# Performance work log

Measured on AMD Instinct MI355X. Metric: run time of the kernel, lower is better.

The kernel has to match this reference:

```python
import jax, jax.numpy as jnp
import numpy as np

B, S, HID = 2, 2048, 1024
NH, DK, DV = 4, 256, 256   # head_k_dim = head_v_dim = 1024 / 4
KSZ = 4                    # conv_size
EPS = 1e-5


def causal_conv1d(x, w):
    # x: [B, S, C] channels-last, w: [C, K] depthwise kernel (torch [C,1,K] squeezed)
    K = w.shape[1]
    Sn = x.shape[1]
    xp = jnp.pad(x, ((0, 0), (K - 1, 0), (0, 0)))
    # cross-correlation with left padding K-1 -> causal: out[t] = sum_j w[:,j] * x[t-(K-1)+j]
    out = xp[:, 0:Sn, :] * w[:, 0]
    for j in range(1, K):
        out = out + xp[:, j:j + Sn, :] * w[:, j]
    return out


def l2norm(x, eps=1e-6):
    return x * jax.lax.rsqrt(jnp.sum(x * x, axis=-1, keepdims=True) + eps)


def rms_norm(x, w, eps=EPS):
    return x * jax.lax.rsqrt(jnp.mean(x * x, axis=-1, keepdims=True) + eps) * w


def delta_rule(q, k, v, beta):
    # q,k: [B,S,H,dk]; v: [B,S,H,dv]; beta: [B,S,H]
    Bn, Sn, Hn, dk = q.shape
    dv = v.shape[-1]
    N = Bn * Hn
    qs = jnp.moveaxis(q, 1, 0).reshape(Sn, N, dk)
    ks = jnp.moveaxis(k, 1, 0).reshape(Sn, N, dk)
    vs = jnp.moveaxis(v, 1, 0).reshape(Sn, N, dv)
    bs = jnp.moveaxis(beta, 1, 0).reshape(Sn, N)

    S0 = jnp.zeros((N, dk, dv), q.dtype)

    def step(St, inp):
        qt, kt, vt, bt = inp
        kS = jnp.einsum('nk,nkv->nv', kt, St)              # k^T S
        St = St + jnp.einsum('nk,nv->nkv', kt, bt[:, None] * (vt - kS))
        ot = jnp.einsum('nk,nkv->nv', qt, St)
        return St, ot

    _, o = jax.lax.scan(step, S0, (qs, ks, vs, bs))        # o: [S, N, dv]
    o = o.reshape(Sn, Bn, Hn, dv)
    return jnp.moveaxis(o, 0, 1)                            # [B,S,H,dv]


def setup_inputs() -> dict:
    key = jax.random.key(0)
    ks = jax.random.split(key, 10)
    w_scale = 2.0 ** (-2.5) * np.sqrt(6.0 / (HID + HID))   # xavier_uniform with gain 2^-2.5
    u = lambda k, shp, s: jax.random.uniform(k, shp, jnp.float32, -s, s)
    return {
        'hidden_states': jax.random.normal(ks[0], (B, S, HID), jnp.float32),
        'Wq': u(ks[1], (HID, NH * DK), w_scale),
        'Wk': u(ks[2], (HID, NH * DK), w_scale),
        'Wv': u(ks[3], (HID, NH * DV), w_scale),
        'Wb': u(ks[4], (HID, NH), w_scale),
        'conv_q': jax.random.normal(ks[5], (NH * DK, KSZ), jnp.float32) * 0.2,
        'conv_k': jax.random.normal(ks[6], (NH * DK, KSZ), jnp.float32) * 0.2,
        'conv_v': jax.random.normal(ks[7], (NH * DV, KSZ), jnp.float32) * 0.2,
        'norm_w': jnp.ones((DV,), jnp.float32),
        'Wo': u(ks[8], (NH * DV, HID), w_scale),
    }


def reference(hidden_states, Wq, Wk, Wv, Wb, conv_q, conv_k, conv_v, norm_w, Wo):
    q = hidden_states @ Wq                                  # [B,S,key_dim]
    k = hidden_states @ Wk
    v = hidden_states @ Wv
    q = causal_conv1d(q, conv_q)
    k = causal_conv1d(k, conv_k)
    v = causal_conv1d(v, conv_v)
    q = jax.nn.silu(q).reshape(B, S, NH, DK)
    k = jax.nn.silu(k).reshape(B, S, NH, DK)
    v = jax.nn.silu(v).reshape(B, S, NH, DV)
    beta = jax.nn.sigmoid(hidden_states @ Wb)               # [B,S,H]
    q = l2norm(q)
    k = l2norm(k)
    o = delta_rule(q, k, v, beta)                           # [B,S,H,dv]
    o = rms_norm(o, norm_w)
    o = o.reshape(B, S, NH * DV) @ Wo                       # [B,S,HID]
    return o
```

## Files before the change

kernel.cpp:

```cpp
#include <hip/hip_runtime.h>
#include <math.h>

#define BB   2
#define SS   2048
#define HIDD 1024
#define ROWS 4096
#define NCH  32
#define CH   64

typedef unsigned short u16t;
typedef unsigned int   u32t;

typedef __attribute__((ext_vector_type(8))) short bf16x8;
typedef __attribute__((ext_vector_type(4))) float f32x4;

__device__ __forceinline__ float bf2f(u16t u) { return __uint_as_float(((u32t)u) << 16); }
__device__ __forceinline__ u16t f2bf(float f) {
    u32t b = __float_as_uint(f);
    return (u16t)((b + 0x7FFFu + ((b >> 16) & 1u)) >> 16);
}
__device__ __forceinline__ float lo_bf(u32t u) { return __uint_as_float(u << 16); }
__device__ __forceinline__ float hi_bf(u32t u) { return __uint_as_float(u & 0xFFFF0000u); }

__device__ __forceinline__ float waveReduceSum(float v) {
#pragma unroll
    for (int m = 1; m < 64; m <<= 1) v += __shfl_xor(v, m, 64);
    return v;
}

__device__ __forceinline__ void gload16(const void* g, void* l) {
    __builtin_amdgcn_global_load_lds(
        (const __attribute__((address_space(1))) unsigned int*)g,
        (__attribute__((address_space(3))) unsigned int*)l, 16, 0, 0);
}

#define MFMA(a, b, c) __builtin_amdgcn_mfma_f32_16x16x32_bf16(a, b, c, 0, 0, 0)

__global__ __launch_bounds__(256) void f2bf_kernel(const float* __restrict__ in,
                                                   u16t* __restrict__ out) {
    const size_t idx = ((size_t)blockIdx.x * 256 + threadIdx.x) * 8;
    float4 a = *(const float4*)&in[idx];
    float4 b = *(const float4*)&in[idx + 4];
    ushort4 o1, o2;
    o1.x = f2bf(a.x); o1.y = f2bf(a.y); o1.z = f2bf(a.z); o1.w = f2bf(a.w);
    o2.x = f2bf(b.x); o2.y = f2bf(b.y); o2.z = f2bf(b.z); o2.w = f2bf(b.w);
    *(ushort4*)&out[idx] = o1;
    *(ushort4*)&out[idx + 4] = o2;
}

__global__ __launch_bounds__(256) void transpose_w(const float* __restrict__ W,
                                                   u16t* __restrict__ WT) {
    __shared__ u16t tile[64][65];
    const int t = threadIdx.x;
    const int r0 = blockIdx.y * 64, c0 = blockIdx.x * 64;
    const int lr = t >> 2, lc4 = (t & 3) * 16;
#pragma unroll
    for (int m = 0; m < 4; ++m) {
        float4 v = *(const float4*)&W[(size_t)(r0 + lr) * 1024 + c0 + lc4 + m * 4];
        tile[lr][lc4 + m * 4 + 0] = f2bf(v.x);
        tile[lr][lc4 + m * 4 + 1] = f2bf(v.y);
        tile[lr][lc4 + m * 4 + 2] = f2bf(v.z);
        tile[lr][lc4 + m * 4 + 3] = f2bf(v.w);
    }
    __syncthreads();
#pragma unroll
    for (int m = 0; m < 16; ++m)
        WT[(size_t)(c0 + lr) * 1024 + r0 + lc4 + m] = tile[lc4 + m][lr];
}

__global__ __launch_bounds__(256) void gemm_mfma(const u16t* __restrict__ A,
                                                 const u16t* __restrict__ BT,
                                                 float* __restrict__ Cf,
                                                 u16t* __restrict__ Cb, int obf,
                                                 int M, int N, int K) {
    __shared__ u16t As[128 * 64];
    __shared__ u16t Bs[128 * 64];
    const int t = threadIdx.x, l = t & 63, w = t >> 6;
    const int wr = w >> 1, wc = w & 1;
    const int rowBase = blockIdx.y * 128, colBase = blockIdx.x * 128;
    const int l15 = l & 15, g4 = l >> 4;

    const int srow = l >> 3;
    const int sj = (l & 7) ^ srow;
    const u16t* aSrc = A + (size_t)(rowBase + srow) * K + sj * 8;
    const u16t* bSrc = BT + (size_t)(colBase + srow) * K + sj * 8;

    f32x4 acc[4][4];
#pragma unroll
    for (int i = 0; i < 4; ++i)
#pragma unroll
        for (int j = 0; j < 4; ++j) acc[i][j] = (f32x4){0.f, 0.f, 0.f, 0.f};

    for (int k0 = 0; k0 < K; k0 += 64) {
#pragma unroll
        for (int i = 0; i < 4; ++i) {
            const int rb = (i * 4 + w) * 8;
            gload16(aSrc + (size_t)rb * K + k0, &As[rb * 64]);
            gload16(bSrc + (size_t)rb * K + k0, &Bs[rb * 64]);
        }
        __syncthreads();
#pragma unroll
        for (int kh = 0; kh < 2; ++kh) {
            bf16x8 aF[4], bF[4];
#pragma unroll
            for (int mi = 0; mi < 4; ++mi) {
                const int row = wr * 64 + mi * 16 + l15;
                const int phys = (kh * 4 + g4) ^ (row & 7);
                aF[mi] = *(const bf16x8*)&As[row * 64 + phys * 8];
            }
#pragma unroll
            for (int ni = 0; ni < 4; ++ni) {
                const int row = wc * 64 + ni * 16 + l15;
                const int phys = (kh * 4 + g4) ^ (row & 7);
                bF[ni] = *(const bf16x8*)&Bs[row * 64 + phys * 8];
            }
#pragma unroll
            for (int mi = 0; mi < 4; ++mi)
#pragma unroll
                for (int ni = 0; ni < 4; ++ni)
                    acc[mi][ni] = MFMA(aF[mi], bF[ni], acc[mi][ni]);
        }
        __syncthreads();
    }
#pragma unroll
    for (int mi = 0; mi < 4; ++mi)
#pragma unroll
        for (int ni = 0; ni < 4; ++ni)
#pragma unroll
            for (int rg = 0; rg < 4; ++rg) {
                const int row = rowBase + wr * 64 + mi * 16 + g4 * 4 + rg;
                const int col = colBase + wc * 64 + ni * 16 + l15;
                const float v = acc[mi][ni][rg];
                if (obf) Cb[(size_t)row * N + col] = f2bf(v);
                else     Cf[(size_t)row * N + col] = v;
            }
}

__global__ __launch_bounds__(256) void beta_kernel(const float* __restrict__ X,
                                                   const float* __restrict__ Wb,
                                                   float* __restrict__ beta) {
    const int gw   = (blockIdx.x * blockDim.x + threadIdx.x) >> 6;
    const int lane = threadIdx.x & 63;
    if (gw >= ROWS) return;
    const float* x = X + (size_t)gw * HIDD;
    float a0 = 0.f, a1 = 0.f, a2 = 0.f, a3 = 0.f;
#pragma unroll
    for (int i = 0; i < 4; ++i) {
        const int k = lane * 16 + i * 4;
        float4 xv = *(const float4*)&x[k];
        float4 w0 = *(const float4*)&Wb[(size_t)(k + 0) * 4];
        float4 w1 = *(const float4*)&Wb[(size_t)(k + 1) * 4];
        float4 w2 = *(const float4*)&Wb[(size_t)(k + 2) * 4];
        float4 w3 = *(const float4*)&Wb[(size_t)(k + 3) * 4];
        a0 += xv.x * w0.x + xv.y * w1.x + xv.z * w2.x + xv.w * w3.x;
        a1 += xv.x * w0.y + xv.y * w1.y + xv.z * w2.y + xv.w * w3.y;
        a2 += xv.x * w0.z + xv.y * w1.z + xv.z * w2.z + xv.w * w3.z;
        a3 += xv.x * w0.w + xv.y * w1.w + xv.z * w2.w + xv.w * w3.w;
    }
    a0 = waveReduceSum(a0); a1 = waveReduceSum(a1);
    a2 = waveReduceSum(a2); a3 = waveReduceSum(a3);
    if (lane == 0) {
        float4 o = make_float4(1.f / (1.f + expf(-a0)), 1.f / (1.f + expf(-a1)),
                               1.f / (1.f + expf(-a2)), 1.f / (1.f + expf(-a3)));
        *(float4*)&beta[(size_t)gw * 4] = o;
    }
}

__global__ __launch_bounds__(256) void conv_bf16(const u16t* __restrict__ in,
                                                 const float* __restrict__ w,
                                                 u16t* __restrict__ out, int doL2) {
    const int gw   = (blockIdx.x * blockDim.x + threadIdx.x) >> 6;
    const int lane = threadIdx.x & 63;
    const int r = gw >> 2;
    const int h = gw & 3;
    const int b = r >> 11;
    const int s = r & 2047;
    const int c4 = h * 256 + lane * 4;

    const float4 wr0 = *(const float4*)&w[(size_t)(c4 + 0) * 4];
    const float4 wr1 = *(const float4*)&w[(size_t)(c4 + 1) * 4];
    const float4 wr2 = *(const float4*)&w[(size_t)(c4 + 2) * 4];
    const float4 wr3 = *(const float4*)&w[(size_t)(c4 + 3) * 4];

    const size_t rowB = (size_t)(b << 11);
    float x0[4] = {0, 0, 0, 0}, x1[4] = {0, 0, 0, 0}, x2[4] = {0, 0, 0, 0}, x3[4];
    ushort4 u;
    if (s >= 3) { u = *(const ushort4*)&in[(rowB + s - 3) * HIDD + c4];
        x0[0] = bf2f(u.x); x0[1] = bf2f(u.y); x0[2] = bf2f(u.z); x0[3] = bf2f(u.w); }
    if (s >= 2) { u = *(const ushort4*)&in[(rowB + s - 2) * HIDD + c4];
        x1[0] = bf2f(u.x); x1[1] = bf2f(u.y); x1[2] = bf2f(u.z); x1[3] = bf2f(u.w); }
    if (s >= 1) { u = *(const ushort4*)&in[(rowB + s - 1) * HIDD + c4];
        x2[0] = bf2f(u.x); x2[1] = bf2f(u.y); x2[2] = bf2f(u.z); x2[3] = bf2f(u.w); }
    u = *(const ushort4*)&in[(rowB + s) * HIDD + c4];
    x3[0] = bf2f(u.x); x3[1] = bf2f(u.y); x3[2] = bf2f(u.z); x3[3] = bf2f(u.w);

    float y0 = wr0.x * x0[0] + wr0.y * x1[0] + wr0.z * x2[0] + wr0.w * x3[0];
    float y1 = wr1.x * x0[1] + wr1.y * x1[1] + wr1.z * x2[1] + wr1.w * x3[1];
    float y2 = wr2.x * x0[2] + wr2.y * x1[2] + wr2.z * x2[2] + wr2.w * x3[2];
    float y3 = wr3.x * x0[3] + wr3.y * x1[3] + wr3.z * x2[3] + wr3.w * x3[3];

    y0 = y0 / (1.f + expf(-y0)); y1 = y1 / (1.f + expf(-y1));
    y2 = y2 / (1.f + expf(-y2)); y3 = y3 / (1.f + expf(-y3));

    if (doL2) {
        float ss = y0 * y0 + y1 * y1 + y2 * y2 + y3 * y3;
        ss = waveReduceSum(ss);
        float sc = rsqrtf(ss + 1e-6f);
        y0 *= sc; y1 *= sc; y2 *= sc; y3 *= sc;
    }
    ushort4 o;
    o.x = f2bf(y0); o.y = f2bf(y1); o.z = f2bf(y2); o.w = f2bf(y3);
    *(ushort4*)&out[(size_t)r * HIDD + c4] = o;
}

__global__ __launch_bounds__(256) void conv_k_chunk(const u16t* __restrict__ pre,
                                                    const float* __restrict__ w,
                                                    u16t* __restrict__ rowout,
                                                    u16t* __restrict__ trout) {
    const int t = threadIdx.x;
    const int bh = blockIdx.x >> 5, c = blockIdx.x & 31;
    const int b = bh >> 2, h = bh & 3;
    const int i = t >> 2, g = t & 3;
    const int s = c * 64 + i;
    const size_t row = (size_t)b * 2048 + s;
    const int ch0 = h * 256 + g * 64;
    const int cloc = g * 64;
    float y[64];
#pragma unroll
    for (int m = 0; m < 8; ++m) {
        const int cm = ch0 + m * 8;
        uint4 x3 = *(const uint4*)&pre[row * 1024 + cm];
        uint4 x2 = (s >= 1) ? *(const uint4*)&pre[(row - 1) * 1024 + cm] : make_uint4(0, 0, 0, 0);
        uint4 x1 = (s >= 2) ? *(const uint4*)&pre[(row - 2) * 1024 + cm] : make_uint4(0, 0, 0, 0);
        uint4 x0 = (s >= 3) ? *(const uint4*)&pre[(row - 3) * 1024 + cm] : make_uint4(0, 0, 0, 0);
        u32t c0[4] = {x0.x, x0.y, x0.z, x0.w};
        u32t c1[4] = {x1.x, x1.y, x1.z, x1.w};
        u32t c2[4] = {x2.x, x2.y, x2.z, x2.w};
        u32t c3[4] = {x3.x, x3.y, x3.z, x3.w};
#pragma unroll
        for (int p = 0; p < 4; ++p) {
            const int ch = m * 8 + p * 2;
            float4 wA = *(const float4*)&w[(size_t)(ch0 + ch) * 4];
            float4 wB = *(const float4*)&w[(size_t)(ch0 + ch + 1) * 4];
            float ya = wA.x * lo_bf(c0[p]) + wA.y * lo_bf(c1[p]) + wA.z * lo_bf(c2[p]) + wA.w * lo_bf(c3[p]);
            float yb = wB.x * hi_bf(c0[p]) + wB.y * hi_bf(c1[p]) + wB.z * hi_bf(c2[p]) + wB.w * hi_bf(c3[p]);
            ya = ya / (1.f + expf(-ya));
            yb = yb / (1.f + expf(-yb));
            y[ch] = ya; y[ch + 1] = yb;
        }
    }
    float ss = 0.f;
#pragma unroll
    for (int e = 0; e < 64; ++e) ss += y[e] * y[e];
    ss += __shfl_xor(ss, 1);
    ss += __shfl_xor(ss, 2);
    const float sc = rsqrtf(ss + 1e-6f);
#pragma unroll
    for (int m = 0; m < 8; ++m) {
        uint4 o;
        u32t* op = (u32t*)&o;
#pragma unroll
        for (int p = 0; p < 4; ++p) {
            u16t a = f2bf(y[m * 8 + p * 2] * sc);
            u16t bb2 = f2bf(y[m * 8 + p * 2 + 1] * sc);
            op[p] = (u32t)a | ((u32t)bb2 << 16);
        }
        *(uint4*)&rowout[row * 1024 + ch0 + m * 8] = o;
    }
#pragma unroll
    for (int e = 0; e < 64; ++e)
        trout[((size_t)bh * 256 + cloc + e) * 2048 + s] = f2bf(y[e] * sc);
}

__global__ __launch_bounds__(256) void prep_kernel(const u16t* __restrict__ qcb,
                                                   const u16t* __restrict__ kcb,
                                                   const float* __restrict__ beta,
                                                   u16t* __restrict__ Tghi,
                                                   u16t* __restrict__ Tglo,
                                                   u16t* __restrict__ Agb) {
    __shared__ float KT[256][68];
    __shared__ float QT[256][68];
    __shared__ float Af[64][68];
    const int t = threadIdx.x;
    const int bhc = blockIdx.x;
    const int bh = bhc >> 5, c = bhc & 31;
    const int b = bh >> 2, h = bh & 3;
    const int tb = b * SS + c * CH;

    {
        const int i = t & 63, rb = t >> 6;
        const u16t* kg = kcb + (size_t)(tb + i) * HIDD + h * 256 + rb * 64;
        const u16t* qg = qcb + (size_t)(tb + i) * HIDD + h * 256 + rb * 64;
#pragma unroll
        for (int m = 0; m < 8; ++m) {
            uint4 kv = ((const uint4*)kg)[m];
            uint4 qv = ((const uint4*)qg)[m];
            u32t kw[4] = {kv.x, kv.y, kv.z, kv.w};
            u32t qw[4] = {qv.x, qv.y, qv.z, qv.w};
#pragma unroll
            for (int n = 0; n < 4; ++n) {
                int rr = rb * 64 + m * 8 + n * 2;
                KT[rr][i]     = lo_bf(kw[n]);
                KT[rr + 1][i] = hi_bf(kw[n]);
                QT[rr][i]     = lo_bf(qw[n]);
                QT[rr + 1][i] = hi_bf(qw[n]);
            }
        }
    }
    __syncthreads();

    const int it = t & 63, jb = t >> 6;
    float kk[16], qk[16];
#pragma unroll
    for (int m = 0; m < 16; ++m) { kk[m] = 0.f; qk[m] = 0.f; }
#pragma unroll 2
    for (int r = 0; r < 256; ++r) {
        float ki = KT[r][it];
        float qi = QT[r][it];
        float4 ka = *(const float4*)&KT[r][jb * 16 + 0];
        float4 kb = *(const float4*)&KT[r][jb * 16 + 4];
        float4 kc = *(const float4*)&KT[r][jb * 16 + 8];
        float4 kd = *(const float4*)&KT[r][jb * 16 + 12];
        float kj[16] = {ka.x, ka.y, ka.z, ka.w, kb.x, kb.y, kb.z, kb.w,
                        kc.x, kc.y, kc.z, kc.w, kd.x, kd.y, kd.z, kd.w};
#pragma unroll
        for (int m = 0; m < 16; ++m) { kk[m] += ki * kj[m]; qk[m] += qi * kj[m]; }
    }

    const float bta = beta[(size_t)(tb + it) * 4 + h];
    u16t* ag = Agb + (size_t)bhc * 4096 + (size_t)it * 64 + jb * 16;
#pragma unroll
    for (int m = 0; m < 16; ++m) {
        int j = jb * 16 + m;
        Af[it][j] = (j < it) ? bta * kk[m] : 0.f;
    }
#pragma unroll
    for (int m4 = 0; m4 < 4; ++m4) {
        ushort4 o;
        o.x = f2bf((jb * 16 + m4 * 4 + 0 <= it) ? qk[m4 * 4 + 0] : 0.f);
        o.y = f2bf((jb * 16 + m4 * 4 + 1 <= it) ? qk[m4 * 4 + 1] : 0.f);
        o.z = f2bf((jb * 16 + m4 * 4 + 2 <= it) ? qk[m4 * 4 + 2] : 0.f);
        o.w = f2bf((jb * 16 + m4 * 4 + 3 <= it) ? qk[m4 * 4 + 3] : 0.f);
        *(ushort4*)&ag[m4 * 4] = o;
    }
    __syncthreads();

    if (t < 64) {
        const int ccol = t;
        float tc[64];
#pragma unroll
        for (int j = 0; j < 64; ++j) tc[j] = (j == ccol) ? 1.f : 0.f;
#pragma unroll
        for (int i = 1; i < 64; ++i) {
            float a = 0.f;
#pragma unroll
            for (int j = 0; j < i; ++j) a += Af[i][j] * tc[j];
            tc[i] -= a;
        }
        u16t* th = Tghi + (size_t)bhc * 4096;
        u16t* tl = Tglo + (size_t)bhc * 4096;
#pragma unroll
        for (int i = 0; i < 64; ++i) {
            u16t hi = f2bf(tc[i]);
            th[i * 64 + ccol] = hi;
            tl[i * 64 + ccol] = f2bf(tc[i] - bf2f(hi));
        }
    }
}

__global__ __launch_bounds__(256) void scan_mfma(const u16t* __restrict__ qcb,
                                                 const u16t* __restrict__ kcb,
                                                 const u16t* __restrict__ ktr,
                                                 const u16t* __restrict__ vcb,
                                                 const float* __restrict__ beta,
                                                 const u16t* __restrict__ TghiG,
                                                 const u16t* __restrict__ TgloG,
                                                 const u16t* __restrict__ AgbG,
                                                 u16t* __restrict__ o_raw) {
    __shared__ u16t Kr[64 * 256];
    __shared__ u16t Qr[64 * 256];
    __shared__ u16t Kc[256 * 64];
    __shared__ u16t Shi[16 * 256];
    __shared__ u16t Slo[16 * 256];
    __shared__ u16t Thi[64 * 64];
    __shared__ u16t Tlo[64 * 64];
    __shared__ u16t Atb[64 * 64];
    __shared__ u16t Rhi[16 * 64];
    __shared__ u16t Rlo[16 * 64];
    __shared__ u16t Uhi[16 * 64];
    __shared__ u16t Ulo[16 * 64];

    const int t = threadIdx.x, l = t & 63, w = t >> 6;
    const int bh = blockIdx.x >> 4, vt = blockIdx.x & 15;
    const int b = bh >> 2, h = bh & 3;
    const int vcol0 = vt * 16;
    const int vlow = l & 15, g4 = l >> 4;
    const int td0 = 16 * w + 4 * g4;

    for (int i = t; i < 16 * 256; i += 256) { Shi[i] = 0; Slo[i] = 0; }
    f32x4 sf[4];
#pragma unroll
    for (int q = 0; q < 4; ++q) sf[q] = (f32x4){0.f, 0.f, 0.f, 0.f};
    __syncthreads();

    for (int c = 0; c < NCH; ++c) {
        const int trow0 = b * 2048 + c * 64;
        const int bhc = bh * 32 + c;

        {
            const int lr2 = l >> 5, s5 = l & 31;
            const u16t* kB = kcb + (size_t)trow0 * 1024 + h * 256;
            const u16t* qB = qcb + (size_t)trow0 * 1024 + h * 256;
#pragma unroll
            for (int i = 0; i < 8; ++i) {
                const int tb2 = (i * 4 + w) * 2;
                const int tr = tb2 + lr2;
                const int j = s5 ^ (tr & 7);
                gload16(kB + (size_t)tr * 1024 + j * 8, &Kr[tb2 * 256]);
                gload16(qB + (size_t)tr * 1024 + j * 8, &Qr[tb2 * 256]);
            }
            const int lr8 = l >> 3, s3 = l & 7;
#pragma unroll
            for (int i = 0; i < 8; ++i) {
                const int rb = (i * 4 + w) * 8;
                const int r = rb + lr8;
                const int j = s3 ^ lr8;
                gload16(ktr + ((size_t)bh * 256 + r) * 2048 + (c * 64 + j * 8), &Kc[rb * 64]);
            }
#pragma unroll
            for (int i = 0; i < 2; ++i) {
                const int rb = (i * 4 + w) * 8;
                const int r = rb + lr8;
                const int j = s3 ^ lr8;
                gload16(TghiG + (size_t)bhc * 4096 + r * 64 + j * 8, &Thi[rb * 64]);
                gload16(TgloG + (size_t)bhc * 4096 + r * 64 + j * 8, &Tlo[rb * 64]);
                gload16(AgbG + (size_t)bhc * 4096 + r * 64 + j * 8, &Atb[rb * 64]);
            }
        }
        float vf[4], bta[4];
#pragma unroll
        for (int rg = 0; rg < 4; ++rg) {
            vf[rg]  = bf2f(vcb[(size_t)(trow0 + td0 + rg) * 1024 + h * 256 + vcol0 + vlow]);
            bta[rg] = beta[(size_t)(trow0 + td0 + rg) * 4 + h];
        }
        __syncthreads();

        f32x4 Wacc = (f32x4){0.f, 0.f, 0.f, 0.f};
        f32x4 O1   = (f32x4){0.f, 0.f, 0.f, 0.f};
        const int arow = 16 * w + vlow;
#pragma unroll
        for (int ks = 0; ks < 8; ++ks) {
            const int physA = (4 * ks + g4) ^ (arow & 7);
            const int physB = (4 * ks + g4) ^ (vlow & 7);
            bf16x8 aK = *(const bf16x8*)&Kr[arow * 256 + physA * 8];
            bf16x8 aQ = *(const bf16x8*)&Qr[arow * 256 + physA * 8];
            bf16x8 bH = *(const bf16x8*)&Shi[vlow * 256 + physB * 8];
            bf16x8 bL = *(const bf16x8*)&Slo[vlow * 256 + physB * 8];
            Wacc = MFMA(aK, bH, Wacc); Wacc = MFMA(aK, bL, Wacc);
            O1   = MFMA(aQ, bH, O1);   O1   = MFMA(aQ, bL, O1);
        }
        {
            u16t rh[4], rl[4];
#pragma unroll
            for (int rg = 0; rg < 4; ++rg) {
                float rv = bta[rg] * (vf[rg] - Wacc[rg]);
                u16t hi = f2bf(rv);
                rh[rg] = hi;
                rl[rg] = f2bf(rv - bf2f(hi));
            }
            const int tslot = 2 * w + (g4 >> 1);
            const int base = vlow * 64 + ((tslot ^ (vlow & 7)) << 3) + ((g4 & 1) << 2);
            uint2 ph, pl;
            ph.x = (u32t)rh[0] | ((u32t)rh[1] << 16); ph.y = (u32t)rh[2] | ((u32t)rh[3] << 16);
            pl.x = (u32t)rl[0] | ((u32t)rl[1] << 16); pl.y = (u32t)rl[2] | ((u32t)rl[3] << 16);
            *(uint2*)&Rhi[base] = ph;
            *(uint2*)&Rlo[base] = pl;
        }
        __syncthreads();

        f32x4 Uacc = (f32x4){0.f, 0.f, 0.f, 0.f};
#pragma unroll
        for (int ks = 0; ks < 2; ++ks) {
            const int physA = (4 * ks + g4) ^ (arow & 7);
            const int physB = (4 * ks + g4) ^ (vlow & 7);
            bf16x8 aH = *(const bf16x8*)&Thi[arow * 64 + physA * 8];
            bf16x8 aL = *(const bf16x8*)&Tlo[arow * 64 + physA * 8];
            bf16x8 bH = *(const bf16x8*)&Rhi[vlow * 64 + physB * 8];
            bf16x8 bL = *(const bf16x8*)&Rlo[vlow * 64 + physB * 8];
            Uacc = MFMA(aH, bH, Uacc);
            Uacc = MFMA(aH, bL, Uacc);
            Uacc = MFMA(aL, bH, Uacc);
        }
        {
            u16t uh[4], ul[4];
#pragma unroll
            for (int rg = 0; rg < 4; ++rg) {
                u16t hi = f2bf(Uacc[rg]);
                uh[rg] = hi;
                ul[rg] = f2bf(Uacc[rg] - bf2f(hi));
            }
            const int tslot = 2 * w + (g4 >> 1);
            const int base = vlow * 64 + ((tslot ^ (vlow & 7)) << 3) + ((g4 & 1) << 2);
            uint2 ph, pl;
            ph.x = (u32t)uh[0] | ((u32t)uh[1] << 16); ph.y = (u32t)uh[2] | ((u32t)uh[3] << 16);
            pl.x = (u32t)ul[0] | ((u32t)ul[1] << 16); pl.y = (u32t)ul[2] | ((u32t)ul[3] << 16);
            *(uint2*)&Uhi[base] = ph;
            *(uint2*)&Ulo[base] = pl;
        }
        __syncthreads();

        bf16x8 uhf[2], ulf[2];
#pragma unroll
        for (int ks = 0; ks < 2; ++ks) {
            const int physB = (4 * ks + g4) ^ (vlow & 7);
            uhf[ks] = *(const bf16x8*)&Uhi[vlow * 64 + physB * 8];
            ulf[ks] = *(const bf16x8*)&Ulo[vlow * 64 + physB * 8];
        }
        f32x4 Oacc = O1;
#pragma unroll
        for (int ks = 0; ks < 2; ++ks) {
            const int physA = (4 * ks + g4) ^ (arow & 7);
            bf16x8 aA = *(const bf16x8*)&Atb[arow * 64 + physA * 8];
            Oacc = MFMA(aA, uhf[ks], Oacc);
            Oacc = MFMA(aA, ulf[ks], Oacc);
        }
#pragma unroll
        for (int rg = 0; rg < 4; ++rg)
            o_raw[(size_t)(trow0 + td0 + rg) * 1024 + h * 256 + vcol0 + vlow] = f2bf(Oacc[rg]);

#pragma unroll
        for (int q = 0; q < 4; ++q) {
            const int rrow = 64 * w + 16 * q + vlow;
#pragma unroll
            for (int ks = 0; ks < 2; ++ks) {
                const int physA = (4 * ks + g4) ^ (rrow & 7);
                bf16x8 aC = *(const bf16x8*)&Kc[rrow * 64 + physA * 8];
                sf[q] = MFMA(aC, uhf[ks], sf[q]);
                sf[q] = MFMA(aC, ulf[ks], sf[q]);
            }
        }
#pragma unroll
        for (int q = 0; q < 4; ++q) {
            u16t sh[4], sl[4];
#pragma unroll
            for (int rg = 0; rg < 4; ++rg) {
                u16t hi = f2bf(sf[q][rg]);
                sh[rg] = hi;
                sl[rg] = f2bf(sf[q][rg] - bf2f(hi));
            }
            const int rslot = 8 * w + 2 * q + (g4 >> 1);
            const int base = vlow * 256 + ((rslot ^ (vlow & 7)) << 3) + ((g4 & 1) << 2);
            uint2 ph, pl;
            ph.x = (u32t)sh[0] | ((u32t)sh[1] << 16); ph.y = (u32t)sh[2] | ((u32t)sh[3] << 16);
            pl.x = (u32t)sl[0] | ((u32t)sl[1] << 16); pl.y = (u32t)sl[2] | ((u32t)sl[3] << 16);
            *(uint2*)&Shi[base] = ph;
            *(uint2*)&Slo[base] = pl;
        }
        __syncthreads();
    }
}

__global__ __launch_bounds__(256) void rms_kernel(const u16t* __restrict__ in,
                                                  const float* __restrict__ w,
                                                  u16t* __restrict__ out) {
    const int gw   = (blockIdx.x * blockDim.x + threadIdx.x) >> 6;
    const int lane = threadIdx.x & 63;
    const int r = gw >> 2;
    const int h = gw & 3;
    const size_t base = (size_t)r * HIDD + h * 256 + lane * 4;
    ushort4 xv = *(const ushort4*)&in[base];
    float x0 = bf2f(xv.x), x1 = bf2f(xv.y), x2 = bf2f(xv.z), x3 = bf2f(xv.w);
    float ss = x0 * x0 + x1 * x1 + x2 * x2 + x3 * x3;
    ss = waveReduceSum(ss);
    const float sc = rsqrtf(ss * (1.0f / 256.0f) + 1e-5f);
    float4 wv = *(const float4*)&w[lane * 4];
    ushort4 o;
    o.x = f2bf(x0 * sc * wv.x); o.y = f2bf(x1 * sc * wv.y);
    o.z = f2bf(x2 * sc * wv.z); o.w = f2bf(x3 * sc * wv.w);
    *(ushort4*)&out[base] = o;
}

extern "C" void kernel_launch(void* const* d_in, const int* in_sizes, int n_in,
                              void* d_out, int out_size, void* d_ws, size_t ws_size,
                              hipStream_t stream) {
    const float* X      = (const float*)d_in[0];
    const float* Wq     = (const float*)d_in[1];
    const float* Wk     = (const float*)d_in[2];
    const float* Wv     = (const float*)d_in[3];
    const float* Wb     = (const float*)d_in[4];
    const float* conv_q = (const float*)d_in[5];
    const float* conv_k = (const float*)d_in[6];
    const float* conv_v = (const float*)d_in[7];
    const float* norm_w = (const float*)d_in[8];
    const float* Wo     = (const float*)d_in[9];
    float* out = (float*)d_out;

    char* W8 = (char*)d_ws;
    const size_t MB = 1u << 20;
    u16t* Xbf   = (u16t*)(W8 + 0 * MB);
    u16t* o_raw = Xbf;
    u16t* qpre  = (u16t*)(W8 + 8 * MB);
    u16t* o_nrm = qpre;
    u16t* kpre  = (u16t*)(W8 + 16 * MB);
    u16t* Tghi  = (u16t*)(W8 + 16 * MB);
    u16t* Tglo  = (u16t*)(W8 + 18 * MB);
    u16t* Agb   = (u16t*)(W8 + 20 * MB);
    u16t* vpre  = (u16t*)(W8 + 24 * MB);
    u16t* ktr   = (u16t*)(W8 + 24 * MB);
    u16t* WqT   = (u16t*)(W8 + 32 * MB);
    u16t* qcb   = (u16t*)(W8 + 32 * MB);
    u16t* WkT   = (u16t*)(W8 + 40 * MB);
    u16t* kcb   = (u16t*)(W8 + 40 * MB);
    u16t* WvT   = (u16t*)(W8 + 48 * MB);
    u16t* vcb   = (u16t*)(W8 + 48 * MB);
    u16t* WoT   = (u16t*)(W8 + 56 * MB);
    float* betab = (float*)(W8 + 58 * MB);

    dim3 tgrid(16, 16);
    f2bf_kernel<<<2048, 256, 0, stream>>>(X, Xbf);
    transpose_w<<<tgrid, 256, 0, stream>>>(Wq, WqT);
    transpose_w<<<tgrid, 256, 0, stream>>>(Wk, WkT);
    transpose_w<<<tgrid, 256, 0, stream>>>(Wv, WvT);
    transpose_w<<<tgrid, 256, 0, stream>>>(Wo, WoT);

    dim3 ggrid(HIDD / 128, ROWS / 128);
    gemm_mfma<<<ggrid, 256, 0, stream>>>(Xbf, WqT, nullptr, qpre, 1, ROWS, HIDD, HIDD);
    gemm_mfma<<<ggrid, 256, 0, stream>>>(Xbf, WkT, nullptr, kpre, 1, ROWS, HIDD, HIDD);
    gemm_mfma<<<ggrid, 256, 0, stream>>>(Xbf, WvT, nullptr, vpre, 1, ROWS, HIDD, HIDD);
    beta_kernel<<<ROWS / 4, 256, 0, stream>>>(X, Wb, betab);

    conv_bf16<<<ROWS, 256, 0, stream>>>(vpre, conv_v, vcb, 0);
    conv_bf16<<<ROWS, 256, 0, stream>>>(qpre, conv_q, qcb, 1);
    conv_k_chunk<<<256, 256, 0, stream>>>(kpre, conv_k, kcb, ktr);

    prep_kernel<<<256, 256, 0, stream>>>(qcb, kcb, betab, Tghi, Tglo, Agb);
    scan_mfma<<<128, 256, 0, stream>>>(qcb, kcb, ktr, vcb, betab, Tghi, Tglo, Agb, o_raw);

    rms_kernel<<<ROWS, 256, 0, stream>>>(o_raw, norm_w, o_nrm);
    gemm_mfma<<<ggrid, 256, 0, stream>>>(o_nrm, WoT, out, nullptr, 0, ROWS, HIDD, HIDD);
}
```

Measured before the change: 316.4 us.

## Prefetch scan operands into registers and merge QKV projections into one GEMM

The chunked delta-rule scan kernel no longer stages K, Q, K-transpose, T and A tiles through shared memory. Each wave now loads its MFMA fragments straight into registers and prefetches the next chunk's operands during the current chunk's compute, so global latency overlaps with MFMA work and several barriers' worth of LDS traffic go away. The three Q/K/V projection GEMMs become one launch with 768 blocks by passing plane strides, relying on the three transposed weights and outputs sitting 8 MB apart. This raises register pressure (launch_bounds 256,1) and depends on that buffer layout staying contiguous.

```diff
diff --git a/kernel.cpp b/kernel.cpp
--- a/kernel.cpp
+++ b/kernel.cpp
@@ -72,7 +72,8 @@
                                                  const u16t* __restrict__ BT,
                                                  float* __restrict__ Cf,
                                                  u16t* __restrict__ Cb, int obf,
-                                                 int M, int N, int K) {
+                                                 int M, int N, int K,
+                                                 size_t bStrideP, size_t cStrideP) {
     __shared__ u16t As[128 * 64];
     __shared__ u16t Bs[128 * 64];
     const int t = threadIdx.x, l = t & 63, w = t >> 6;
@@ -80,10 +81,13 @@
     const int rowBase = blockIdx.y * 128, colBase = blockIdx.x * 128;
     const int l15 = l & 15, g4 = l >> 4;
 
+    const int bplane = colBase >> 10;
+    const int bcol = colBase & 1023;
+
     const int srow = l >> 3;
     const int sj = (l & 7) ^ srow;
     const u16t* aSrc = A + (size_t)(rowBase + srow) * K + sj * 8;
-    const u16t* bSrc = BT + (size_t)(colBase + srow) * K + sj * 8;
+    const u16t* bSrc = BT + (size_t)bplane * bStrideP + (size_t)(bcol + srow) * K + sj * 8;
 
     f32x4 acc[4][4];
 #pragma unroll
@@ -130,9 +134,10 @@
             for (int rg = 0; rg < 4; ++rg) {
                 const int row = rowBase + wr * 64 + mi * 16 + g4 * 4 + rg;
                 const int col = colBase + wc * 64 + ni * 16 + l15;
+                const int plane = col >> 10, cc = col & 1023;
                 const float v = acc[mi][ni][rg];
-                if (obf) Cb[(size_t)row * N + col] = f2bf(v);
-                else     Cf[(size_t)row * N + col] = v;
+                if (obf) Cb[(size_t)plane * cStrideP + (size_t)row * 1024 + cc] = f2bf(v);
+                else     Cf[(size_t)plane * cStrideP + (size_t)row * 1024 + cc] = v;
             }
 }
 
@@ -368,23 +373,17 @@
     }
 }
 
-__global__ __launch_bounds__(256) void scan_mfma(const u16t* __restrict__ qcb,
-                                                 const u16t* __restrict__ kcb,
-                                                 const u16t* __restrict__ ktr,
-                                                 const u16t* __restrict__ vcb,
-                                                 const float* __restrict__ beta,
-                                                 const u16t* __restrict__ TghiG,
-                                                 const u16t* __restrict__ TgloG,
-                                                 const u16t* __restrict__ AgbG,
-                                                 u16t* __restrict__ o_raw) {
-    __shared__ u16t Kr[64 * 256];
-    __shared__ u16t Qr[64 * 256];
-    __shared__ u16t Kc[256 * 64];
+__global__ __launch_bounds__(256, 1) void scan_mfma(const u16t* __restrict__ qcb,
+                                                    const u16t* __restrict__ kcb,
+                                                    const u16t* __restrict__ ktr,
+                                                    const u16t* __restrict__ vcb,
+                                                    const float* __restrict__ beta,
+                                                    const u16t* __restrict__ TghiG,
+                                                    const u16t* __restrict__ TgloG,
+                                                    const u16t* __restrict__ AgbG,
+                                                    u16t* __restrict__ o_raw) {
     __shared__ u16t Shi[16 * 256];
     __shared__ u16t Slo[16 * 256];
-    __shared__ u16t Thi[64 * 64];
-    __shared__ u16t Tlo[64 * 64];
-    __shared__ u16t Atb[64 * 64];
     __shared__ u16t Rhi[16 * 64];
     __shared__ u16t Rlo[16 * 64];
     __shared__ u16t Uhi[16 * 64];
@@ -395,150 +394,146 @@
     const int b = bh >> 2, h = bh & 3;
     const int vcol0 = vt * 16;
     const int vlow = l & 15, g4 = l >> 4;
-    const int td0 = 16 * w + 4 * g4;
 
     for (int i = t; i < 16 * 256; i += 256) { Shi[i] = 0; Slo[i] = 0; }
     f32x4 sf[4];
 #pragma unroll
     for (int q = 0; q < 4; ++q) sf[q] = (f32x4){0.f, 0.f, 0.f, 0.f};
+
+    bf16x8 kf[8], qf[8], tfh[2], tfl[2], af[2], kcf[8];
+    u16t vfb[4];
+    float bta[4];
+
+    auto loadKQ = [&](int c) {
+        const size_t rb = (size_t)(b * 2048 + c * 64 + 16 * w + vlow) * 1024 + h * 256 + g4 * 8;
+#pragma unroll
+        for (int ks = 0; ks < 8; ++ks) {
+            kf[ks] = *(const bf16x8*)(kcb + rb + ks * 32);
+            qf[ks] = *(const bf16x8*)(qcb + rb + ks * 32);
+        }
+    };
+    auto loadVB = [&](int c) {
+        const int r0 = b * 2048 + c * 64 + 16 * w + 4 * g4;
+#pragma unroll
+        for (int rg = 0; rg < 4; ++rg) {
+            vfb[rg] = vcb[(size_t)(r0 + rg) * 1024 + h * 256 + vcol0 + vlow];
+            bta[rg] = beta[(size_t)(r0 + rg) * 4 + h];
+        }
+    };
+    auto loadT = [&](int c) {
+        const size_t tb2 = (size_t)(bh * 32 + c) * 4096 + (size_t)(16 * w + vlow) * 64 + g4 * 8;
+        tfh[0] = *(const bf16x8*)(TghiG + tb2);
+        tfh[1] = *(const bf16x8*)(TghiG + tb2 + 32);
+        tfl[0] = *(const bf16x8*)(TgloG + tb2);
+        tfl[1] = *(const bf16x8*)(TgloG + tb2 + 32);
+    };
+    auto loadA = [&](int c) {
+        const size_t tb2 = (size_t)(bh * 32 + c) * 4096 + (size_t)(16 * w + vlow) * 64 + g4 * 8;
+        af[0] = *(const bf16x8*)(AgbG + tb2);
+        af[1] = *(const bf16x8*)(AgbG + tb2 + 32);
+    };
+    auto loadKC = [&](int c) {
+        const size_t cb2 = ((size_t)bh * 256 + 64 * w + vlow) * 2048 + c * 64 + g4 * 8;
+#pragma unroll
+        for (int q2 = 0; q2 < 4; ++q2) {
+            kcf[q2 * 2 + 0] = *(const bf16x8*)(ktr + cb2 + (size_t)(16 * q2) * 2048);
+            kcf[q2 * 2 + 1] = *(const bf16x8*)(ktr + cb2 + (size_t)(16 * q2) * 2048 + 32);
+        }
+    };
+
+    loadKQ(0); loadVB(0); loadT(0); loadA(0); loadKC(0);
     __syncthreads();
 
     for (int c = 0; c < NCH; ++c) {
+        const int cn = (c + 1 < NCH) ? c + 1 : c;
         const int trow0 = b * 2048 + c * 64;
-        const int bhc = bh * 32 + c;
-
-        {
-            const int lr2 = l >> 5, s5 = l & 31;
-            const u16t* kB = kcb + (size_t)trow0 * 1024 + h * 256;
-            const u16t* qB = qcb + (size_t)trow0 * 1024 + h * 256;
-#pragma unroll
-            for (int i = 0; i < 8; ++i) {
-                const int tb2 = (i * 4 + w) * 2;
-                const int tr = tb2 + lr2;
-                const int j = s5 ^ (tr & 7);
-                gload16(kB + (size_t)tr * 1024 + j * 8, &Kr[tb2 * 256]);
-                gload16(qB + (size_t)tr * 1024 + j * 8, &Qr[tb2 * 256]);
-            }
-            const int lr8 = l >> 3, s3 = l & 7;
-#pragma unroll
-            for (int i = 0; i < 8; ++i) {
-                const int rb = (i * 4 + w) * 8;
-                const int r = rb + lr8;
-                const int j = s3 ^ lr8;
-                gload16(ktr + ((size_t)bh * 256 + r) * 2048 + (c * 64 + j * 8), &Kc[rb * 64]);
-            }
-#pragma unroll
-            for (int i = 0; i < 2; ++i) {
-                const int rb = (i * 4 + w) * 8;
-                const int r = rb + lr8;
-                const int j = s3 ^ lr8;
-                gload16(TghiG + (size_t)bhc * 4096 + r * 64 + j * 8, &Thi[rb * 64]);
-                gload16(TgloG + (size_t)bhc * 4096 + r * 64 + j * 8, &Tlo[rb * 64]);
-                gload16(AgbG + (size_t)bhc * 4096 + r * 64 + j * 8, &Atb[rb * 64]);
-            }
-        }
-        float vf[4], bta[4];
-#pragma unroll
-        for (int rg = 0; rg < 4; ++rg) {
-            vf[rg]  = bf2f(vcb[(size_t)(trow0 + td0 + rg) * 1024 + h * 256 + vcol0 + vlow]);
-            bta[rg] = beta[(size_t)(trow0 + td0 + rg) * 4 + h];
-        }
-        __syncthreads();
 
         f32x4 Wacc = (f32x4){0.f, 0.f, 0.f, 0.f};
         f32x4 O1   = (f32x4){0.f, 0.f, 0.f, 0.f};
-        const int arow = 16 * w + vlow;
 #pragma unroll
         for (int ks = 0; ks < 8; ++ks) {
-            const int physA = (4 * ks + g4) ^ (arow & 7);
-            const int physB = (4 * ks + g4) ^ (vlow & 7);
-            bf16x8 aK = *(const bf16x8*)&Kr[arow * 256 + physA * 8];
-            bf16x8 aQ = *(const bf16x8*)&Qr[arow * 256 + physA * 8];
-            bf16x8 bH = *(const bf16x8*)&Shi[vlow * 256 + physB * 8];
-            bf16x8 bL = *(const bf16x8*)&Slo[vlow * 256 + physB * 8];
-            Wacc = MFMA(aK, bH, Wacc); Wacc = MFMA(aK, bL, Wacc);
-            O1   = MFMA(aQ, bH, O1);   O1   = MFMA(aQ, bL, O1);
+            const int pb = (((ks * 4 + g4) ^ (vlow & 7)) << 3);
+            bf16x8 bH = *(const bf16x8*)&Shi[vlow * 256 + pb];
+            bf16x8 bL = *(const bf16x8*)&Slo[vlow * 256 + pb];
+            Wacc = MFMA(kf[ks], bH, Wacc); Wacc = MFMA(kf[ks], bL, Wacc);
+            O1   = MFMA(qf[ks], bH, O1);   O1   = MFMA(qf[ks], bL, O1);
         }
         {
-            u16t rh[4], rl[4];
-#pragma unroll
-            for (int rg = 0; rg < 4; ++rg) {
-                float rv = bta[rg] * (vf[rg] - Wacc[rg]);
-                u16t hi = f2bf(rv);
-                rh[rg] = hi;
-                rl[rg] = f2bf(rv - bf2f(hi));
-            }
             const int tslot = 2 * w + (g4 >> 1);
             const int base = vlow * 64 + ((tslot ^ (vlow & 7)) << 3) + ((g4 & 1) << 2);
+            u16t rh[4], rl[4];
+#pragma unroll
+            for (int rg = 0; rg < 4; ++rg) {
+                float rv = bta[rg] * (bf2f(vfb[rg]) - Wacc[rg]);
+                rh[rg] = f2bf(rv);
+                rl[rg] = f2bf(rv - bf2f(rh[rg]));
+            }
             uint2 ph, pl;
             ph.x = (u32t)rh[0] | ((u32t)rh[1] << 16); ph.y = (u32t)rh[2] | ((u32t)rh[3] << 16);
             pl.x = (u32t)rl[0] | ((u32t)rl[1] << 16); pl.y = (u32t)rl[2] | ((u32t)rl[3] << 16);
             *(uint2*)&Rhi[base] = ph;
             *(uint2*)&Rlo[base] = pl;
         }
+        loadKQ(cn);
+        loadVB(cn);
         __syncthreads();
 
         f32x4 Uacc = (f32x4){0.f, 0.f, 0.f, 0.f};
 #pragma unroll
         for (int ks = 0; ks < 2; ++ks) {
-            const int physA = (4 * ks + g4) ^ (arow & 7);
-            const int physB = (4 * ks + g4) ^ (vlow & 7);
-            bf16x8 aH = *(const bf16x8*)&Thi[arow * 64 + physA * 8];
-            bf16x8 aL = *(const bf16x8*)&Tlo[arow * 64 + physA * 8];
-            bf16x8 bH = *(const bf16x8*)&Rhi[vlow * 64 + physB * 8];
-            bf16x8 bL = *(const bf16x8*)&Rlo[vlow * 64 + physB * 8];
-            Uacc = MFMA(aH, bH, Uacc);
-            Uacc = MFMA(aH, bL, Uacc);
-            Uacc = MFMA(aL, bH, Uacc);
+            const int pb = (((ks * 4 + g4) ^ (vlow & 7)) << 3);
+            bf16x8 bH = *(const bf16x8*)&Rhi[vlow * 64 + pb];
+            bf16x8 bL = *(const bf16x8*)&Rlo[vlow * 64 + pb];
+            Uacc = MFMA(tfh[ks], bH, Uacc);
+            Uacc = MFMA(tfh[ks], bL, Uacc);
+            Uacc = MFMA(tfl[ks], bH, Uacc);
         }
         {
-            u16t uh[4], ul[4];
-#pragma unroll
-            for (int rg = 0; rg < 4; ++rg) {
-                u16t hi = f2bf(Uacc[rg]);
-                uh[rg] = hi;
-                ul[rg] = f2bf(Uacc[rg] - bf2f(hi));
-            }
             const int tslot = 2 * w + (g4 >> 1);
             const int base = vlow * 64 + ((tslot ^ (vlow & 7)) << 3) + ((g4 & 1) << 2);
+            u16t uh[4], ul[4];
+#pragma unroll
+            for (int rg = 0; rg < 4; ++rg) {
+                uh[rg] = f2bf(Uacc[rg]);
+                ul[rg] = f2bf(Uacc[rg] - bf2f(uh[rg]));
+            }
             uint2 ph, pl;
             ph.x = (u32t)uh[0] | ((u32t)uh[1] << 16); ph.y = (u32t)uh[2] | ((u32t)uh[3] << 16);
             pl.x = (u32t)ul[0] | ((u32t)ul[1] << 16); pl.y = (u32t)ul[2] | ((u32t)ul[3] << 16);
             *(uint2*)&Uhi[base] = ph;
             *(uint2*)&Ulo[base] = pl;
         }
+        loadT(cn);
         __syncthreads();
 
         bf16x8 uhf[2], ulf[2];
 #pragma unroll
         for (int ks = 0; ks < 2; ++ks) {
-            const int physB = (4 * ks + g4) ^ (vlow & 7);
-            uhf[ks] = *(const bf16x8*)&Uhi[vlow * 64 + physB * 8];
-            ulf[ks] = *(const bf16x8*)&Ulo[vlow * 64 + physB * 8];
+            const int pb = (((ks * 4 + g4) ^ (vlow & 7)) << 3);
+            uhf[ks] = *(const bf16x8*)&Uhi[vlow * 64 + pb];
+            ulf[ks] = *(const bf16x8*)&Ulo[vlow * 64 + pb];
         }
         f32x4 Oacc = O1;
 #pragma unroll
         for (int ks = 0; ks < 2; ++ks) {
-            const int physA = (4 * ks + g4) ^ (arow & 7);
-            bf16x8 aA = *(const bf16x8*)&Atb[arow * 64 + physA * 8];
-            Oacc = MFMA(aA, uhf[ks], Oacc);
-            Oacc = MFMA(aA, ulf[ks], Oacc);
+            Oacc = MFMA(af[ks], uhf[ks], Oacc);
+            Oacc = MFMA(af[ks], ulf[ks], Oacc);
         }
 #pragma unroll
         for (int rg = 0; rg < 4; ++rg)
-            o_raw[(size_t)(trow0 + td0 + rg) * 1024 + h * 256 + vcol0 + vlow] = f2bf(Oacc[rg]);
+            o_raw[(size_t)(trow0 + 16 * w + 4 * g4 + rg) * 1024 + h * 256 + vcol0 + vlow] = f2bf(Oacc[rg]);
+        loadA(cn);
 
 #pragma unroll
         for (int q = 0; q < 4; ++q) {
-            const int rrow = 64 * w + 16 * q + vlow;
 #pragma unroll
             for (int ks = 0; ks < 2; ++ks) {
-                const int physA = (4 * ks + g4) ^ (rrow & 7);
-                bf16x8 aC = *(const bf16x8*)&Kc[rrow * 64 + physA * 8];
-                sf[q] = MFMA(aC, uhf[ks], sf[q]);
-                sf[q] = MFMA(aC, ulf[ks], sf[q]);
-            }
-        }
+                sf[q] = MFMA(kcf[q * 2 + ks], uhf[ks], sf[q]);
+                sf[q] = MFMA(kcf[q * 2 + ks], ulf[ks], sf[q]);
+            }
+        }
+        loadKC(cn);
+
 #pragma unroll
         for (int q = 0; q < 4; ++q) {
             u16t sh[4], sl[4];
@@ -616,6 +611,8 @@
     u16t* WoT   = (u16t*)(W8 + 56 * MB);
     float* betab = (float*)(W8 + 58 * MB);
 
+    const size_t PL = 4194304;
+
     dim3 tgrid(16, 16);
     f2bf_kernel<<<2048, 256, 0, stream>>>(X, Xbf);
     transpose_w<<<tgrid, 256, 0, stream>>>(Wq, WqT);
@@ -623,10 +620,8 @@
     transpose_w<<<tgrid, 256, 0, stream>>>(Wv, WvT);
     transpose_w<<<tgrid, 256, 0, stream>>>(Wo, WoT);
 
-    dim3 ggrid(HIDD / 128, ROWS / 128);
-    gemm_mfma<<<ggrid, 256, 0, stream>>>(Xbf, WqT, nullptr, qpre, 1, ROWS, HIDD, HIDD);
-    gemm_mfma<<<ggrid, 256, 0, stream>>>(Xbf, WkT, nullptr, kpre, 1, ROWS, HIDD, HIDD);
-    gemm_mfma<<<ggrid, 256, 0, stream>>>(Xbf, WvT, nullptr, vpre, 1, ROWS, HIDD, HIDD);
+    gemm_mfma<<<dim3(24, 32), 256, 0, stream>>>(Xbf, WqT, nullptr, qpre, 1,
+                                                ROWS, 3072, HIDD, PL, PL);
     beta_kernel<<<ROWS / 4, 256, 0, stream>>>(X, Wb, betab);
 
     conv_bf16<<<ROWS, 256, 0, stream>>>(vpre, conv_v, vcb, 0);
@@ -637,5 +632,6 @@
     scan_mfma<<<128, 256, 0, stream>>>(qcb, kcb, ktr, vcb, betab, Tghi, Tglo, Agb, o_raw);
 
     rms_kernel<<<ROWS, 256, 0, stream>>>(o_raw, norm_w, o_nrm);
-    gemm_mfma<<<ggrid, 256, 0, stream>>>(o_nrm, WoT, out, nullptr, 0, ROWS, HIDD, HIDD);
-}
+    gemm_mfma<<<dim3(8, 32), 256, 0, stream>>>(o_nrm, WoT, out, nullptr, 0,
+                                               ROWS, HIDD, HIDD, 0, 0);
+}
```

New measurement: 293.9 us. 1.08x faster.
